# Kernel optimization log

Hardware: AMD Instinct MI355X
Metric: run time of the kernel (lower is better)

The kernel has to match this reference:

```python
import jax, jax.numpy as jnp
import numpy as np

BN_EPS = 1e-5


def setup_inputs() -> dict:
    key = jax.random.key(0)
    k = jax.random.split(key, 4)
    B, T, D, H, L = 32, 512, 1024, 1024, 3
    x = jax.random.normal(k[0], (B, T, D), dtype=jnp.float32)
    # Linear weights stored torch-style: out_features x in_features
    W = jax.random.normal(k[1], (L, 2 * H, D), dtype=jnp.float32) * 0.02
    U = jax.random.normal(k[2], (L, 2 * H, H), dtype=jnp.float32) * 0.02
    gamma = jnp.ones((L, 2 * H), dtype=jnp.float32)
    beta = jnp.zeros((L, 2 * H), dtype=jnp.float32)
    run_mean = jax.random.normal(k[3], (L, 2 * H), dtype=jnp.float32) * 0.01
    run_var = jnp.ones((L, 2 * H), dtype=jnp.float32)
    return dict(x=x, W=W, U=U, gamma=gamma, beta=beta,
                run_mean=run_mean, run_var=run_var)


def _ligru_layer(x, W, U, g, b, m, v):
    # x: [B,T,D]; W: [2H,D]; U: [2H,H]
    H = U.shape[1]
    w = jnp.einsum('btd,ed->bte', x, W)            # input projection, [B,T,2H]
    # BatchNorm1d in eval mode: per-channel affine with running stats
    w = (w - m) * (g * jax.lax.rsqrt(v + BN_EPS)) + b

    def step(h, wt):
        gates = wt + h @ U.T                        # [B,2H]
        at, zt = gates[:, :H], gates[:, H:]
        z = jax.nn.sigmoid(zt)
        hcand = jax.nn.relu(at)                     # drop_mask = 1 (eval)
        h = z * h + (1.0 - z) * hcand
        return h, h

    h0 = jnp.zeros((x.shape[0], H), dtype=x.dtype)  # h_init buffer
    _, hs = jax.lax.scan(step, h0, jnp.swapaxes(w, 0, 1))  # [T,B,H]
    return jnp.swapaxes(hs, 0, 1)                   # [B,T,H]


def reference(x, W, U, gamma, beta, run_mean, run_var):
    h_last = []
    for i in range(W.shape[0]):                     # loop over L=3 layers
        x = _ligru_layer(x, W[i], U[i], gamma[i], beta[i],
                         run_mean[i], run_var[i])
        h_last.append(x[:, -1])
    hh = jnp.stack(h_last, axis=1)                  # [B,L,H]
    return x, hh
```

## Files before the change

### kernel.cpp

```cpp
#include <hip/hip_runtime.h>
#include <hip/hip_bf16.h>
#include <stdint.h>

typedef _Float16 f16;
typedef _Float16 f16x8 __attribute__((ext_vector_type(8)));
typedef float f32x4 __attribute__((ext_vector_type(4)));
typedef unsigned long long u64;

#define LDF16X8(p) (*reinterpret_cast<const f16x8*>(p))

__device__ __forceinline__ f16x8 ld_h(const f16* p) {
  union { u64 q[2]; f16x8 v; } u;
  u.q[0] = __hip_atomic_load((const u64*)p,     __ATOMIC_RELAXED, __HIP_MEMORY_SCOPE_AGENT);
  u.q[1] = __hip_atomic_load((const u64*)p + 1, __ATOMIC_RELAXED, __HIP_MEMORY_SCOPE_AGENT);
  return u.v;
}

__global__ __launch_bounds__(256) void k_cvt(const float* __restrict__ in,
                                             f16* __restrict__ out, int n) {
  int i = (blockIdx.x * 256 + threadIdx.x) * 4;
  if (i + 3 < n) {
    float4 v = *reinterpret_cast<const float4*>(in + i);
    out[i + 0] = (f16)v.x; out[i + 1] = (f16)v.y;
    out[i + 2] = (f16)v.z; out[i + 3] = (f16)v.w;
  } else {
    for (; i < n; ++i) out[i] = (f16)in[i];
  }
}

__global__ __launch_bounds__(256) void k_gemm_bn(
    const f16* __restrict__ A,
    const f16* __restrict__ B,
    const float* __restrict__ gamma, const float* __restrict__ beta,
    const float* __restrict__ mean, const float* __restrict__ var,
    f16* __restrict__ out,
    int M, int N, int K) {
  __shared__ f16 Al[4 * 128 * 8];
  __shared__ f16 Bl[4 * 128 * 8];
  const int tid = threadIdx.x;
  const int lane = tid & 63, wid = tid >> 6;
  const int wm = wid >> 1, wn = wid & 1;
  const int row0 = blockIdx.x * 128, col0 = blockIdx.y * 128;

  f32x4 acc[4][4] = {};

  const int sR = tid >> 1;
  const int sk8 = (tid & 1) * 2;

  for (int k0 = 0; k0 < K; k0 += 32) {
    __syncthreads();
    {
      const f16* srcA = A + (size_t)(row0 + sR) * K + k0 + sk8 * 8;
      uint4 a0 = *reinterpret_cast<const uint4*>(srcA);
      uint4 a1 = *reinterpret_cast<const uint4*>(srcA + 8);
      *reinterpret_cast<uint4*>(&Al[(sk8 * 128 + sR) * 8]) = a0;
      *reinterpret_cast<uint4*>(&Al[((sk8 + 1) * 128 + sR) * 8]) = a1;
      const f16* srcB = B + (size_t)(col0 + sR) * K + k0 + sk8 * 8;
      uint4 b0 = *reinterpret_cast<const uint4*>(srcB);
      uint4 b1 = *reinterpret_cast<const uint4*>(srcB + 8);
      *reinterpret_cast<uint4*>(&Bl[(sk8 * 128 + sR) * 8]) = b0;
      *reinterpret_cast<uint4*>(&Bl[((sk8 + 1) * 128 + sR) * 8]) = b1;
    }
    __syncthreads();

    const int k8 = lane >> 4, r16 = lane & 15;
    f16x8 af[4], bfr[4];
#pragma unroll
    for (int m = 0; m < 4; ++m)
      af[m] = LDF16X8(&Al[(k8 * 128 + wm * 64 + m * 16 + r16) * 8]);
#pragma unroll
    for (int n = 0; n < 4; ++n)
      bfr[n] = LDF16X8(&Bl[(k8 * 128 + wn * 64 + n * 16 + r16) * 8]);
#pragma unroll
    for (int m = 0; m < 4; ++m)
#pragma unroll
      for (int n = 0; n < 4; ++n)
        acc[m][n] = __builtin_amdgcn_mfma_f32_16x16x32_f16(af[m], bfr[n], acc[m][n], 0, 0, 0);
  }

#pragma unroll
  for (int n = 0; n < 4; ++n) {
    int col = col0 + wn * 64 + n * 16 + (lane & 15);
    float g = gamma[col], be = beta[col], mu = mean[col], va = var[col];
    float s = g * rsqrtf(va + 1e-5f);
    float sh = be - mu * s;
#pragma unroll
    for (int m = 0; m < 4; ++m) {
#pragma unroll
      for (int r = 0; r < 4; ++r) {
        int row = row0 + wm * 64 + m * 16 + (lane >> 4) * 4 + r;
        out[(size_t)row * N + col] = (f16)(acc[m][n][r] * s + sh);
      }
    }
  }
}

__global__ __launch_bounds__(256) void k_scan(
    const float* __restrict__ U,
    const f16* __restrict__ w,
    f16* __restrict__ hpub,
    f16* __restrict__ xoutH,
    float* __restrict__ xoutF,
    float* __restrict__ hh,
    unsigned* __restrict__ flags,
    int layer, int last, int nwg) {
  __shared__ f16 Ul[16 * 1024];
  __shared__ float gl[2][32][16];

  const int tid = threadIdx.x;
  const int lane = tid & 63, wid = tid >> 6;
  const int mt = wid & 1, kh = wid >> 1;
  const int j0 = blockIdx.x * 8;

  for (int i = tid; i < 16 * 1024; i += 256) {
    int e = i >> 10, k = i & 1023;
    int erow = (e < 8) ? (j0 + e) : (1024 + j0 + e - 8);
    Ul[((k >> 3) * 16 + e) * 8 + (k & 7)] = (f16)U[(size_t)erow * 1024 + k];
  }
  __syncthreads();

  const int cb = tid >> 3;
  const int cj = tid & 7;
  float hreg = 0.f;

  const int r16 = lane & 15, kg4 = lane >> 4;

  float wa = (float)w[(size_t)(cb * 512) * 2048 + j0 + cj];
  float wz = (float)w[(size_t)(cb * 512) * 2048 + 1024 + j0 + cj];

  for (int t = 0; t < 512; ++t) {
    const int cur = t & 1, nxt = cur ^ 1;

    f32x4 acc = {};
    const f16* hbase = hpub + cur * 32768 + (size_t)(mt * 16 + r16) * 1024 + kh * 512 + kg4 * 8;
#pragma unroll
    for (int kk = 0; kk < 16; ++kk) {
      f16x8 a = ld_h(hbase + kk * 32);
      f16x8 b = LDF16X8(&Ul[((kh * 64 + kk * 4 + kg4) * 16 + r16) * 8]);
      acc = __builtin_amdgcn_mfma_f32_16x16x32_f16(a, b, acc, 0, 0, 0);
    }
#pragma unroll
    for (int r = 0; r < 4; ++r)
      gl[kh][mt * 16 + kg4 * 4 + r][r16] = acc[r];
    __syncthreads();

    {
      float apre = gl[0][cb][cj] + gl[1][cb][cj] + wa;
      float zpre = gl[0][cb][8 + cj] + gl[1][cb][8 + cj] + wz;
      float z = 1.f / (1.f + expf(-zpre));
      float hn = z * hreg + (1.f - z) * fmaxf(apre, 0.f);
      hreg = hn;
      f16 hf = (f16)hn;
      unsigned hb = (unsigned)__builtin_bit_cast(unsigned short, hf);
      unsigned nb = __shfl_down(hb, 1, 64);
      if ((cj & 1) == 0)
        __hip_atomic_store((unsigned*)(hpub + nxt * 32768 + cb * 1024 + j0 + cj),
                           hb | (nb << 16), __ATOMIC_RELAXED, __HIP_MEMORY_SCOPE_AGENT);
      size_t xoff = (size_t)(cb * 512 + t) * 1024 + j0 + cj;
      if (last) xoutF[xoff] = hn;
      else      xoutH[xoff] = (f16)hn;
    }

    if (t + 1 < 512) {
      size_t wrow = (size_t)(cb * 512 + t + 1) * 2048;
      wa = (float)w[wrow + j0 + cj];
      wz = (float)w[wrow + 1024 + j0 + cj];
    }

    __syncthreads();
    if (tid == 0)
      __hip_atomic_store(&flags[(size_t)blockIdx.x * 32], t + 1u,
                         __ATOMIC_RELAXED, __HIP_MEMORY_SCOPE_AGENT);
    if (tid < 64) {
      const unsigned tgt = t + 1u;
      for (;;) {
        unsigned a = __hip_atomic_load(&flags[(size_t)tid * 32],
                                       __ATOMIC_RELAXED, __HIP_MEMORY_SCOPE_AGENT);
        unsigned b = __hip_atomic_load(&flags[(size_t)(64 + tid) * 32],
                                       __ATOMIC_RELAXED, __HIP_MEMORY_SCOPE_AGENT);
        if (a >= tgt && b >= tgt) break;
        __builtin_amdgcn_s_sleep(1);
      }
    }
    __syncthreads();
  }

  hh[(size_t)(cb * 3 + layer) * 1024 + j0 + cj] = hreg;
}

extern "C" void kernel_launch(void* const* d_in, const int* in_sizes, int n_in,
                              void* d_out, int out_size, void* d_ws, size_t ws_size,
                              hipStream_t stream) {
  const float* x     = (const float*)d_in[0];
  const float* W     = (const float*)d_in[1];
  const float* U     = (const float*)d_in[2];
  const float* gamma = (const float*)d_in[3];
  const float* beta  = (const float*)d_in[4];
  const float* rmean = (const float*)d_in[5];
  const float* rvar  = (const float*)d_in[6];
  float* outX  = (float*)d_out;
  float* outHH = outX + (size_t)32 * 512 * 1024;

  f16* xb = (f16*)d_out;

  char* ws = (char*)d_ws;
  f16* wbuf = (f16*)(ws);
  f16* Wb   = (f16*)(ws + 67108864);
  f16* hpub = (f16*)(ws + 71303168);
  unsigned* flags = (unsigned*)(ws + 71434240);

  k_cvt<<<16384, 256, 0, stream>>>(x, xb, 16777216);

  for (int l = 0; l < 3; ++l) {
    k_cvt<<<2048, 256, 0, stream>>>(W + (size_t)l * 2097152, Wb, 2097152);
    k_gemm_bn<<<dim3(128, 16), 256, 0, stream>>>(
        xb, Wb, gamma + l * 2048, beta + l * 2048, rmean + l * 2048, rvar + l * 2048,
        wbuf, 16384, 2048, 1024);
    hipMemsetAsync(hpub, 0, 131072, stream);
    hipMemsetAsync(flags, 0, 16384, stream);
    k_scan<<<128, 256, 0, stream>>>(
        U + (size_t)l * 2097152, wbuf, hpub,
        xb, outX, outHH, flags, l, (l == 2) ? 1 : 0, 128);
  }
}
```

Before: 9.618 ms.

## Run recurrent scan on 32 large workgroups with permuted gate-input layout

The persistent scan kernel now uses 32 workgroups of 1024 threads instead of 128 of 256. Each workgroup owns 32 hidden units and holds 128KB of U in LDS. This cuts the number of participants in the per-timestep cross-workgroup flag barrier, so fewer flags are polled. The GEMM epilogue writes its output in a per-workgroup, per-timestep permuted layout so each step's gate inputs are read contiguously, and that prefetch is moved to overlap the flag wait. The trade-off is fewer CUs doing the per-step matvec, and each workgroup does four times the MFMA work per step.

```diff
diff --git a/kernel.cpp b/kernel.cpp
--- a/kernel.cpp
+++ b/kernel.cpp
@@ -33,7 +33,7 @@
     const f16* __restrict__ B,
     const float* __restrict__ gamma, const float* __restrict__ beta,
     const float* __restrict__ mean, const float* __restrict__ var,
-    f16* __restrict__ out,
+    f16* __restrict__ wperm,
     int M, int N, int K) {
   __shared__ f16 Al[4 * 128 * 8];
   __shared__ f16 Bl[4 * 128 * 8];
@@ -80,73 +80,81 @@
 
 #pragma unroll
   for (int n = 0; n < 4; ++n) {
-    int col = col0 + wn * 64 + n * 16 + (lane & 15);
-    float g = gamma[col], be = beta[col], mu = mean[col], va = var[col];
+    int e = col0 + wn * 64 + n * 16 + (lane & 15);
+    float g = gamma[e], be = beta[e], mu = mean[e], va = var[e];
     float s = g * rsqrtf(va + 1e-5f);
     float sh = be - mu * s;
+    int wg_e = (e < 1024) ? (e >> 5) : ((e - 1024) >> 5);
+    int c    = (e & 31) + ((e < 1024) ? 0 : 32);
 #pragma unroll
     for (int m = 0; m < 4; ++m) {
 #pragma unroll
       for (int r = 0; r < 4; ++r) {
         int row = row0 + wm * 64 + m * 16 + (lane >> 4) * 4 + r;
-        out[(size_t)row * N + col] = (f16)(acc[m][n][r] * s + sh);
+        int cb = row >> 9, tt = row & 511;
+        wperm[(((size_t)wg_e * 512 + tt) * 32 + cb) * 64 + c] =
+            (f16)(acc[m][n][r] * s + sh);
       }
     }
   }
 }
 
-__global__ __launch_bounds__(256) void k_scan(
+__global__ __launch_bounds__(1024, 1) void k_scan(
     const float* __restrict__ U,
-    const f16* __restrict__ w,
+    const f16* __restrict__ wperm,
     f16* __restrict__ hpub,
     f16* __restrict__ xoutH,
     float* __restrict__ xoutF,
     float* __restrict__ hh,
     unsigned* __restrict__ flags,
-    int layer, int last, int nwg) {
-  __shared__ f16 Ul[16 * 1024];
-  __shared__ float gl[2][32][16];
+    int layer, int last) {
+  extern __shared__ char smem[];
+  f16* Ul  = (f16*)smem;
+  float* gl = (float*)(smem + 131072);
 
   const int tid = threadIdx.x;
   const int lane = tid & 63, wid = tid >> 6;
-  const int mt = wid & 1, kh = wid >> 1;
-  const int j0 = blockIdx.x * 8;
-
-  for (int i = tid; i < 16 * 1024; i += 256) {
+  const int mt = wid & 1, nt = (wid >> 1) & 3, kq = wid >> 3;
+  const int j0 = blockIdx.x * 32;
+  const int r16 = lane & 15, kg4 = lane >> 4;
+
+  for (int i = tid; i < 64 * 1024; i += 1024) {
     int e = i >> 10, k = i & 1023;
-    int erow = (e < 8) ? (j0 + e) : (1024 + j0 + e - 8);
-    Ul[((k >> 3) * 16 + e) * 8 + (k & 7)] = (f16)U[(size_t)erow * 1024 + k];
+    int erow = (e < 32) ? (j0 + e) : (1024 + j0 + e - 32);
+    Ul[((k >> 3) * 64 + e) * 8 + (k & 7)] = (f16)U[(size_t)erow * 1024 + k];
   }
   __syncthreads();
 
-  const int cb = tid >> 3;
-  const int cj = tid & 7;
+  const int cb = tid >> 5;
+  const int cj = tid & 31;
   float hreg = 0.f;
 
-  const int r16 = lane & 15, kg4 = lane >> 4;
-
-  float wa = (float)w[(size_t)(cb * 512) * 2048 + j0 + cj];
-  float wz = (float)w[(size_t)(cb * 512) * 2048 + 1024 + j0 + cj];
+  float wa, wz;
+  {
+    size_t base = ((size_t)(blockIdx.x * 512 + 0) * 32 + cb) * 64;
+    wa = (float)wperm[base + cj];
+    wz = (float)wperm[base + 32 + cj];
+  }
 
   for (int t = 0; t < 512; ++t) {
     const int cur = t & 1, nxt = cur ^ 1;
 
     f32x4 acc = {};
-    const f16* hbase = hpub + cur * 32768 + (size_t)(mt * 16 + r16) * 1024 + kh * 512 + kg4 * 8;
+    const f16* hbase = hpub + cur * 32768 + (size_t)(mt * 16 + r16) * 1024 + kq * 512 + kg4 * 8;
 #pragma unroll
     for (int kk = 0; kk < 16; ++kk) {
       f16x8 a = ld_h(hbase + kk * 32);
-      f16x8 b = LDF16X8(&Ul[((kh * 64 + kk * 4 + kg4) * 16 + r16) * 8]);
+      f16x8 b = LDF16X8(&Ul[((kq * 64 + kk * 4 + kg4) * 64 + nt * 16 + r16) * 8]);
       acc = __builtin_amdgcn_mfma_f32_16x16x32_f16(a, b, acc, 0, 0, 0);
     }
 #pragma unroll
     for (int r = 0; r < 4; ++r)
-      gl[kh][mt * 16 + kg4 * 4 + r][r16] = acc[r];
+      gl[(kq * 32 + mt * 16 + kg4 * 4 + r) * 64 + nt * 16 + r16] = acc[r];
     __syncthreads();
 
     {
-      float apre = gl[0][cb][cj] + gl[1][cb][cj] + wa;
-      float zpre = gl[0][cb][8 + cj] + gl[1][cb][8 + cj] + wz;
+      float apre = gl[cb * 64 + cj]        + gl[(32 + cb) * 64 + cj]        + wa;
+      float zpre = gl[cb * 64 + 32 + cj]   + gl[(32 + cb) * 64 + 32 + cj]   + wz;
       float z = 1.f / (1.f + expf(-zpre));
       float hn = z * hreg + (1.f - z) * fmaxf(apre, 0.f);
       hreg = hn;
@@ -161,26 +169,20 @@
       else      xoutH[xoff] = (f16)hn;
     }
 
-    if (t + 1 < 512) {
-      size_t wrow = (size_t)(cb * 512 + t + 1) * 2048;
-      wa = (float)w[wrow + j0 + cj];
-      wz = (float)w[wrow + 1024 + j0 + cj];
-    }
-
     __syncthreads();
     if (tid == 0)
       __hip_atomic_store(&flags[(size_t)blockIdx.x * 32], t + 1u,
                          __ATOMIC_RELAXED, __HIP_MEMORY_SCOPE_AGENT);
-    if (tid < 64) {
+    if (t + 1 < 512) {
+      size_t base = ((size_t)(blockIdx.x * 512 + t + 1) * 32 + cb) * 64;
+      wa = (float)wperm[base + cj];
+      wz = (float)wperm[base + 32 + cj];
+    }
+    if (tid < 32) {
       const unsigned tgt = t + 1u;
-      for (;;) {
-        unsigned a = __hip_atomic_load(&flags[(size_t)tid * 32],
-                                       __ATOMIC_RELAXED, __HIP_MEMORY_SCOPE_AGENT);
-        unsigned b = __hip_atomic_load(&flags[(size_t)(64 + tid) * 32],
-                                       __ATOMIC_RELAXED, __HIP_MEMORY_SCOPE_AGENT);
-        if (a >= tgt && b >= tgt) break;
+      while (__hip_atomic_load(&flags[(size_t)tid * 32], __ATOMIC_RELAXED,
+                               __HIP_MEMORY_SCOPE_AGENT) < tgt)
         __builtin_amdgcn_s_sleep(1);
-      }
     }
     __syncthreads();
   }
@@ -204,9 +206,9 @@
   f16* xb = (f16*)d_out;
 
   char* ws = (char*)d_ws;
-  f16* wbuf = (f16*)(ws);
-  f16* Wb   = (f16*)(ws + 67108864);
-  f16* hpub = (f16*)(ws + 71303168);
+  f16* wperm = (f16*)(ws);
+  f16* Wb    = (f16*)(ws + 67108864);
+  f16* hpub  = (f16*)(ws + 71303168);
   unsigned* flags = (unsigned*)(ws + 71434240);
 
   k_cvt<<<16384, 256, 0, stream>>>(x, xb, 16777216);
@@ -215,11 +217,11 @@
     k_cvt<<<2048, 256, 0, stream>>>(W + (size_t)l * 2097152, Wb, 2097152);
     k_gemm_bn<<<dim3(128, 16), 256, 0, stream>>>(
         xb, Wb, gamma + l * 2048, beta + l * 2048, rmean + l * 2048, rvar + l * 2048,
-        wbuf, 16384, 2048, 1024);
+        wperm, 16384, 2048, 1024);
     hipMemsetAsync(hpub, 0, 131072, stream);
-    hipMemsetAsync(flags, 0, 16384, stream);
-    k_scan<<<128, 256, 0, stream>>>(
-        U + (size_t)l * 2097152, wbuf, hpub,
-        xb, outX, outHH, flags, l, (l == 2) ? 1 : 0, 128);
-  }
-}
+    hipMemsetAsync(flags, 0, 4096, stream);
+    k_scan<<<32, 1024, 147456, stream>>>(
+        U + (size_t)l * 2097152, wperm, hpub,
+        xb, outX, outHH, flags, l, (l == 2) ? 1 : 0);
+  }
+}
```

New measurement: 23.87 ms. 2.48x slower.
